# Performance work log

Hardware: AMD Instinct MI355X
Metric: run time of the kernel (lower is better)

## Reference

```python
import jax, jax.numpy as jnp
import numpy as np

V = 50257  # output_size (vocab)
H = 1024   # hidden_size


def setup_inputs() -> dict:
    key = jax.random.key(0)
    ks = jax.random.split(key, 10)
    s = 1.0 / np.sqrt(H)
    return {
        "x": jax.random.randint(ks[0], (1,), 0, V),
        "hidden": jax.random.normal(ks[1], (1, 1, H), dtype=jnp.float32),
        "cell_state": jax.random.normal(ks[2], (1, 1, H), dtype=jnp.float32),
        # learned parameters
        "emb": jax.random.normal(ks[3], (V, H), dtype=jnp.float32),
        "w_ih": jax.random.uniform(ks[4], (4 * H, H), jnp.float32, -s, s),
        "w_hh": jax.random.uniform(ks[5], (4 * H, H), jnp.float32, -s, s),
        "b_ih": jax.random.uniform(ks[6], (4 * H,), jnp.float32, -s, s),
        "b_hh": jax.random.uniform(ks[7], (4 * H,), jnp.float32, -s, s),
        "fc_w": jax.random.uniform(ks[8], (V, H), jnp.float32, -s, s),
        "fc_b": jax.random.uniform(ks[9], (V,), jnp.float32, -s, s),
    }


def reference(x, hidden, cell_state, emb, w_ih, w_hh, b_ih, b_hh, fc_w, fc_b):
    # embedding lookup: [1, H]
    e = emb[x]
    h = hidden[0]      # [1, H]
    c = cell_state[0]  # [1, H]
    # single LSTM step, PyTorch gate order (i, f, g, o)
    gates = e @ w_ih.T + b_ih + h @ w_hh.T + b_hh  # [1, 4H]
    i, f, g, o = jnp.split(gates, 4, axis=-1)
    i = jax.nn.sigmoid(i)
    f = jax.nn.sigmoid(f)
    g = jnp.tanh(g)
    o = jax.nn.sigmoid(o)
    c_new = f * c + i * g
    h_new = o * jnp.tanh(c_new)
    # fc + log-softmax over vocab: [1, V]
    logp = jax.nn.log_softmax(h_new @ fc_w.T + fc_b, axis=1)
    return logp, h_new[None], c_new[None]
```

## Files before the change

### kernel.cpp

```cpp
#include <hip/hip_runtime.h>
#include <hip/hip_bf16.h>
#include <math.h>

#define V 50257
#define H 1024
#define NB_FC 1024
#define NWAVES (NB_FC * 4)

__global__ __launch_bounds__(256) void lstm_kernel(
    const int* __restrict__ x,
    const float* __restrict__ hidden,
    const float* __restrict__ cell,
    const float* __restrict__ emb,
    const float* __restrict__ w_ih,
    const float* __restrict__ w_hh,
    const float* __restrict__ b_ih,
    const float* __restrict__ b_hh,
    float* __restrict__ out)
{
    const int k = blockIdx.x;
    const int t = threadIdx.x;
    const float* e = emb + (size_t)x[0] * H;

    const int idx = t * 4;
    const float4 ev = *(const float4*)(e + idx);
    const float4 hv = *(const float4*)(hidden + idx);

    float p[8];
#pragma unroll
    for (int g = 0; g < 4; ++g) {
        const float4 wi = *(const float4*)(w_ih + (size_t)(g * H + k) * H + idx);
        const float4 wh = *(const float4*)(w_hh + (size_t)(g * H + k) * H + idx);
        p[2 * g]     = wi.x * ev.x + wi.y * ev.y + wi.z * ev.z + wi.w * ev.w;
        p[2 * g + 1] = wh.x * hv.x + wh.y * hv.y + wh.z * hv.z + wh.w * hv.w;
    }

#pragma unroll
    for (int j = 0; j < 8; ++j) {
#pragma unroll
        for (int off = 32; off; off >>= 1)
            p[j] += __shfl_down(p[j], off, 64);
    }

    __shared__ float red[8][4];
    const int wave = t >> 6, lane = t & 63;
    if (lane == 0) {
#pragma unroll
        for (int j = 0; j < 8; ++j) red[j][wave] = p[j];
    }
    __syncthreads();

    if (t == 0) {
        float s[8];
#pragma unroll
        for (int j = 0; j < 8; ++j)
            s[j] = red[j][0] + red[j][1] + red[j][2] + red[j][3];
        const float gi = s[0] + s[1] + b_ih[k]         + b_hh[k];
        const float gf = s[2] + s[3] + b_ih[H + k]     + b_hh[H + k];
        const float gg = s[4] + s[5] + b_ih[2 * H + k] + b_hh[2 * H + k];
        const float go = s[6] + s[7] + b_ih[3 * H + k] + b_hh[3 * H + k];

        const float i_g = 1.0f / (1.0f + expf(-gi));
        const float f_g = 1.0f / (1.0f + expf(-gf));
        const float g_g = tanhf(gg);
        const float o_g = 1.0f / (1.0f + expf(-go));

        const float c_new = f_g * cell[k] + i_g * g_g;
        const float h_new = o_g * tanhf(c_new);

        out[V + k]     = h_new;
        out[V + H + k] = c_new;
    }
}

__global__ __launch_bounds__(256) void fc_lse_kernel(
    const float* __restrict__ fc_w,
    const float* __restrict__ fc_b,
    const float* __restrict__ h_new,
    float* __restrict__ logits,
    float2* __restrict__ partials)
{
    const int wave = threadIdx.x >> 6;
    const int lane = threadIdx.x & 63;
    const int wid = blockIdx.x * 4 + wave;

    float4 hv[4];
#pragma unroll
    for (int it = 0; it < 4; ++it)
        hv[it] = *(const float4*)(h_new + (it * 64 + lane) * 4);

    float m = -INFINITY, s = 0.0f;

    for (int v = wid * 2; v < V; v += NWAVES * 2) {
        const float* r0 = fc_w + (size_t)v * H;
        const bool two = (v + 1 < V);
        const float* r1 = r0 + (two ? H : 0);

        float a0 = 0.0f, a1 = 0.0f;
#pragma unroll
        for (int it = 0; it < 4; ++it) {
            const int off = (it * 64 + lane) * 4;
            const float4 w0 = *(const float4*)(r0 + off);
            const float4 w1 = *(const float4*)(r1 + off);
            a0 += w0.x * hv[it].x + w0.y * hv[it].y + w0.z * hv[it].z + w0.w * hv[it].w;
            a1 += w1.x * hv[it].x + w1.y * hv[it].y + w1.z * hv[it].z + w1.w * hv[it].w;
        }
#pragma unroll
        for (int off = 1; off < 64; off <<= 1) {
            a0 += __shfl_xor(a0, off, 64);
            a1 += __shfl_xor(a1, off, 64);
        }
        a0 += fc_b[v];
        a1 = two ? (a1 + fc_b[v + 1]) : -INFINITY;

        if (lane == 0) {
            logits[v] = a0;
            if (two) logits[v + 1] = a1;
        }

        const float nm = fmaxf(m, fmaxf(a0, a1));
        s = s * __expf(m - nm) + __expf(a0 - nm) + __expf(a1 - nm);
        m = nm;
    }

    __shared__ float2 pm[4];
    if (lane == 0) pm[wave] = make_float2(m, s);
    __syncthreads();
    if (threadIdx.x == 0) {
        float M = pm[0].x, S = pm[0].y;
#pragma unroll
        for (int i = 1; i < 4; ++i) {
            const float m2 = pm[i].x, s2 = pm[i].y;
            const float nM = fmaxf(M, m2);
            S = S * __expf(M - nM) + s2 * __expf(m2 - nM);
            M = nM;
        }
        partials[blockIdx.x] = make_float2(M, S);
    }
}

__global__ __launch_bounds__(256) void logp_kernel(
    const float* __restrict__ logits,
    const float2* __restrict__ partials,
    float* __restrict__ out)
{
    const int t = threadIdx.x;
    const int lane = t & 63;
    const int wave = t >> 6;

    float m = -INFINITY, s = 0.0f;
#pragma unroll
    for (int i = 0; i < 4; ++i) {
        const float2 p = partials[t * 4 + i];
        const float nm = fmaxf(m, p.x);
        s = s * __expf(m - nm) + p.y * __expf(p.x - nm);
        m = nm;
    }
#pragma unroll
    for (int off = 1; off < 64; off <<= 1) {
        const float om = __shfl_xor(m, off, 64);
        const float os = __shfl_xor(s, off, 64);
        const float nm = fmaxf(m, om);
        s = s * __expf(m - nm) + os * __expf(om - nm);
        m = nm;
    }
    __shared__ float2 red[4];
    __shared__ float sub_s;
    if (lane == 0) red[wave] = make_float2(m, s);
    __syncthreads();
    if (t == 0) {
        float M = red[0].x, S = red[0].y;
#pragma unroll
        for (int i = 1; i < 4; ++i) {
            const float nm2 = fmaxf(M, red[i].x);
            S = S * __expf(M - nm2) + red[i].y * __expf(red[i].x - nm2);
            M = nm2;
        }
        sub_s = M + logf(S);
    }
    __syncthreads();
    const float sub = sub_s;

    const int base = (blockIdx.x * 256 + t) * 4;
    if (base + 3 < V) {
        const float4 l = *(const float4*)(logits + base);
        float4 o;
        o.x = l.x - sub; o.y = l.y - sub; o.z = l.z - sub; o.w = l.w - sub;
        *(float4*)(out + base) = o;
    } else {
#pragma unroll
        for (int j = 0; j < 4; ++j) {
            const int v = base + j;
            if (v < V) out[v] = logits[v] - sub;
        }
    }
}

extern "C" void kernel_launch(void* const* d_in, const int* in_sizes, int n_in,
                              void* d_out, int out_size, void* d_ws, size_t ws_size,
                              hipStream_t stream)
{
    const int*   x      = (const int*)  d_in[0];
    const float* hidden = (const float*)d_in[1];
    const float* cell   = (const float*)d_in[2];
    const float* emb    = (const float*)d_in[3];
    const float* w_ih   = (const float*)d_in[4];
    const float* w_hh   = (const float*)d_in[5];
    const float* b_ih   = (const float*)d_in[6];
    const float* b_hh   = (const float*)d_in[7];
    const float* fc_w   = (const float*)d_in[8];
    const float* fc_b   = (const float*)d_in[9];
    float* out = (float*)d_out;

    float*  logits   = (float*)d_ws;
    float2* partials = (float2*)(logits + ((V + 255) & ~255));

    lstm_kernel<<<H, 256, 0, stream>>>(x, hidden, cell, emb, w_ih, w_hh,
                                       b_ih, b_hh, out);
    fc_lse_kernel<<<NB_FC, 256, 0, stream>>>(fc_w, fc_b, out + V, logits, partials);
    logp_kernel<<<(V + 1023) / 1024, 256, 0, stream>>>(logits, partials, out);
}
```

Before: 45.66 us.

## Fuse log-softmax pass into FC kernel using grid barrier and register-held logits

```diff
diff --git a/kernel.cpp b/kernel.cpp
--- a/kernel.cpp
+++ b/kernel.cpp
@@ -4,8 +4,10 @@
 
 #define V 50257
 #define H 1024
-#define NB_FC 1024
+#define NB_FC 768
 #define NWAVES (NB_FC * 4)
+#define QROWS ((V + 3) / 4)
+#define NITER ((QROWS + NWAVES - 1) / NWAVES)
 
 __global__ __launch_bounds__(256) void lstm_kernel(
     const int* __restrict__ x,
@@ -16,12 +18,14 @@
     const float* __restrict__ w_hh,
     const float* __restrict__ b_ih,
     const float* __restrict__ b_hh,
-    float* __restrict__ out)
+    float* __restrict__ out,
+    int* __restrict__ counter)
 {
     const int k = blockIdx.x;
     const int t = threadIdx.x;
+    if (k == 0 && t == 0) *counter = 0;
+
     const float* e = emb + (size_t)x[0] * H;
-
     const int idx = t * 4;
     const float4 ev = *(const float4*)(e + idx);
     const float4 hv = *(const float4*)(hidden + idx);
@@ -73,15 +77,17 @@
     }
 }
 
-__global__ __launch_bounds__(256) void fc_lse_kernel(
+__global__ __launch_bounds__(256, 3) void fc_lse_kernel(
     const float* __restrict__ fc_w,
     const float* __restrict__ fc_b,
     const float* __restrict__ h_new,
-    float* __restrict__ logits,
-    float2* __restrict__ partials)
+    float* __restrict__ out,
+    float2* __restrict__ partials,
+    int* __restrict__ counter)
 {
-    const int wave = threadIdx.x >> 6;
-    const int lane = threadIdx.x & 63;
+    const int t = threadIdx.x;
+    const int wave = t >> 6;
+    const int lane = t & 63;
     const int wid = blockIdx.x * 4 + wave;
 
     float4 hv[4];
@@ -90,43 +96,80 @@
         hv[it] = *(const float4*)(h_new + (it * 64 + lane) * 4);
 
     float m = -INFINITY, s = 0.0f;
-
-    for (int v = wid * 2; v < V; v += NWAVES * 2) {
-        const float* r0 = fc_w + (size_t)v * H;
-        const bool two = (v + 1 < V);
-        const float* r1 = r0 + (two ? H : 0);
-
-        float a0 = 0.0f, a1 = 0.0f;
-#pragma unroll
-        for (int it = 0; it < 4; ++it) {
-            const int off = (it * 64 + lane) * 4;
-            const float4 w0 = *(const float4*)(r0 + off);
-            const float4 w1 = *(const float4*)(r1 + off);
-            a0 += w0.x * hv[it].x + w0.y * hv[it].y + w0.z * hv[it].z + w0.w * hv[it].w;
-            a1 += w1.x * hv[it].x + w1.y * hv[it].y + w1.z * hv[it].z + w1.w * hv[it].w;
+    float lg[NITER];
+
+#pragma unroll
+    for (int j = 0; j < NITER; ++j) {
+        const int idx = j * NWAVES + wid;
+        float val;
+        if (j == NITER - 1 && idx >= QROWS) {
+            val = -INFINITY;
+        } else {
+            const int base = idx * 4;
+            const bool full = (j < NITER - 1) || (base + 3 < V);
+            const float* r0 = fc_w + (size_t)base * H;
+            const float* r1 = full ? r0 + H     : (base + 1 < V ? r0 + H     : r0);
+            const float* r2 = full ? r0 + 2 * H : (base + 2 < V ? r0 + 2 * H : r0);
+            const float* r3 = full ? r0 + 3 * H : (base + 3 < V ? r0 + 3 * H : r0);
+
+            float a0 = 0.f, a1 = 0.f, a2 = 0.f, a3 = 0.f;
+#pragma unroll
+            for (int it = 0; it < 4; ++it) {
+                const int off = (it * 64 + lane) * 4;
+                const float4 w0 = *(const float4*)(r0 + off);
+                const float4 w1 = *(const float4*)(r1 + off);
+                const float4 w2 = *(const float4*)(r2 + off);
+                const float4 w3 = *(const float4*)(r3 + off);
+                a0 += w0.x * hv[it].x + w0.y * hv[it].y + w0.z * hv[it].z + w0.w * hv[it].w;
+                a1 += w1.x * hv[it].x + w1.y * hv[it].y + w1.z * hv[it].z + w1.w * hv[it].w;
+                a2 += w2.x * hv[it].x + w2.y * hv[it].y + w2.z * hv[it].z + w2.w * hv[it].w;
+                a3 += w3.x * hv[it].x + w3.y * hv[it].y + w3.z * hv[it].z + w3.w * hv[it].w;
+            }
+            float b = (lane & 1) ? a0 : a1;
+            b = __shfl_xor(b, 1, 64);
+            float c = ((lane & 1) ? a1 : a0) + b;
+            float d0 = (lane & 1) ? a2 : a3;
+            d0 = __shfl_xor(d0, 1, 64);
+            float d = ((lane & 1) ? a3 : a2) + d0;
+            float e0 = (lane & 2) ? c : d;
+            e0 = __shfl_xor(e0, 2, 64);
+            float f = ((lane & 2) ? d : c) + e0;
+#pragma unroll
+            for (int off = 4; off < 64; off <<= 1)
+                f += __shfl_xor(f, off, 64);
+
+            float bias;
+            if (full) {
+                const float4 b4 = *(const float4*)(fc_b + base);
+                bias = (lane & 1) ? ((lane & 2) ? b4.w : b4.y)
+                                  : ((lane & 2) ? b4.z : b4.x);
+            } else {
+                const int vr = base + (lane & 3);
+                bias = (vr < V) ? fc_b[vr] : 0.0f;
+            }
+            val = f + bias;
+            if (!full && (base + (lane & 3)) >= V) val = -INFINITY;
         }
-#pragma unroll
-        for (int off = 1; off < 64; off <<= 1) {
-            a0 += __shfl_xor(a0, off, 64);
-            a1 += __shfl_xor(a1, off, 64);
-        }
-        a0 += fc_b[v];
-        a1 = two ? (a1 + fc_b[v + 1]) : -INFINITY;
-
-        if (lane == 0) {
-            logits[v] = a0;
-            if (two) logits[v + 1] = a1;
-        }
-
-        const float nm = fmaxf(m, fmaxf(a0, a1));
-        s = s * __expf(m - nm) + __expf(a0 - nm) + __expf(a1 - nm);
+        lg[j] = val;
+        const float nm = fmaxf(m, val);
+        s = s * __expf(m - nm) + __expf(val - nm);
         m = nm;
     }
 
+#pragma unroll
+    for (int off = 1; off < 64; off <<= 1) {
+        const float om = __shfl_xor(m, off, 64);
+        const float os = __shfl_xor(s, off, 64);
+        const float nm = fmaxf(m, om);
+        s = s * __expf(m - nm) + os * __expf(om - nm);
+        m = nm;
+    }
+
     __shared__ float2 pm[4];
+    __shared__ float subs;
     if (lane == 0) pm[wave] = make_float2(m, s);
     __syncthreads();
-    if (threadIdx.x == 0) {
+    if (t == 0) {
         float M = pm[0].x, S = pm[0].y;
 #pragma unroll
         for (int i = 1; i < 4; ++i) {
@@ -135,64 +178,50 @@
             S = S * __expf(M - nM) + s2 * __expf(m2 - nM);
             M = nM;
         }
-        partials[blockIdx.x] = make_float2(M, S);
-    }
-}
-
-__global__ __launch_bounds__(256) void logp_kernel(
-    const float* __restrict__ logits,
-    const float2* __restrict__ partials,
-    float* __restrict__ out)
-{
-    const int t = threadIdx.x;
-    const int lane = t & 63;
-    const int wave = t >> 6;
-
-    float m = -INFINITY, s = 0.0f;
-#pragma unroll
-    for (int i = 0; i < 4; ++i) {
-        const float2 p = partials[t * 4 + i];
-        const float nm = fmaxf(m, p.x);
-        s = s * __expf(m - nm) + p.y * __expf(p.x - nm);
-        m = nm;
+        partials[blockIdx.x] = make_float2(M, S * 0.0625f);
+        __threadfence();
+        __hip_atomic_fetch_add(counter, 1, __ATOMIC_RELEASE, __HIP_MEMORY_SCOPE_AGENT);
+        while (__hip_atomic_load(counter, __ATOMIC_ACQUIRE, __HIP_MEMORY_SCOPE_AGENT) < NB_FC)
+            __builtin_amdgcn_s_sleep(8);
+    }
+    __syncthreads();
+
+    float mm = -INFINITY, ss = 0.0f;
+#pragma unroll
+    for (int i = 0; i < 3; ++i) {
+        const float2 p = partials[t * 3 + i];
+        const float nm = fmaxf(mm, p.x);
+        ss = ss * __expf(mm - nm) + p.y * __expf(p.x - nm);
+        mm = nm;
     }
 #pragma unroll
     for (int off = 1; off < 64; off <<= 1) {
-        const float om = __shfl_xor(m, off, 64);
-        const float os = __shfl_xor(s, off, 64);
-        const float nm = fmaxf(m, om);
-        s = s * __expf(m - nm) + os * __expf(om - nm);
-        m = nm;
-    }
-    __shared__ float2 red[4];
-    __shared__ float sub_s;
-    if (lane == 0) red[wave] = make_float2(m, s);
+        const float om = __shfl_xor(mm, off, 64);
+        const float os = __shfl_xor(ss, off, 64);
+        const float nm = fmaxf(mm, om);
+        ss = ss * __expf(mm - nm) + os * __expf(om - nm);
+        mm = nm;
+    }
+    if (lane == 0) pm[wave] = make_float2(mm, ss);
     __syncthreads();
     if (t == 0) {
-        float M = red[0].x, S = red[0].y;
+        float M = pm[0].x, S = pm[0].y;
 #pragma unroll
         for (int i = 1; i < 4; ++i) {
-            const float nm2 = fmaxf(M, red[i].x);
-            S = S * __expf(M - nm2) + red[i].y * __expf(red[i].x - nm2);
+            const float nm2 = fmaxf(M, pm[i].x);
+            S = S * __expf(M - nm2) + pm[i].y * __expf(pm[i].x - nm2);
             M = nm2;
         }
-        sub_s = M + logf(S);
-    }
-    __syncthreads();
-    const float sub = sub_s;
-
-    const int base = (blockIdx.x * 256 + t) * 4;
-    if (base + 3 < V) {
-        const float4 l = *(const float4*)(logits + base);
-        float4 o;
-        o.x = l.x - sub; o.y = l.y - sub; o.z = l.z - sub; o.w = l.w - sub;
-        *(float4*)(out + base) = o;
-    } else {
-#pragma unroll
-        for (int j = 0; j < 4; ++j) {
-            const int v = base + j;
-            if (v < V) out[v] = logits[v] - sub;
-        }
+        subs = M + logf(S);
+    }
+    __syncthreads();
+    const float sub = subs;
+
+#pragma unroll
+    for (int j = 0; j < NITER; ++j) {
+        const int idx = j * NWAVES + wid;
+        const int v = idx * 4 + (lane & 3);
+        if (lane < 4 && v < V) out[v] = lg[j] - sub;
     }
 }
 
@@ -212,11 +241,11 @@
     const float* fc_b   = (const float*)d_in[9];
     float* out = (float*)d_out;
 
-    float*  logits   = (float*)d_ws;
-    float2* partials = (float2*)(logits + ((V + 255) & ~255));
+    float2* partials = (float2*)d_ws;
+    int*    counter  = (int*)((char*)d_ws + 8192);
 
     lstm_kernel<<<H, 256, 0, stream>>>(x, hidden, cell, emb, w_ih, w_hh,
-                                       b_ih, b_hh, out);
-    fc_lse_kernel<<<NB_FC, 256, 0, stream>>>(fc_w, fc_b, out + V, logits, partials);
-    logp_kernel<<<(V + 1023) / 1024, 256, 0, stream>>>(logits, partials, out);
+                                       b_ih, b_hh, out, counter);
+    fc_lse_kernel<<<NB_FC, 256, 0, stream>>>(fc_w, fc_b, out + V, out,
+                                             partials, counter);
 }
```

After: 160.3 us. 251% more time.
